# Kernel optimization log

Measured on AMD Instinct MI355X. Metric: run time of the kernel, lower is better.

The kernel has to match this reference:

```python
import jax, jax.numpy as jnp
import numpy as np

B, N, DIM, H = 2, 2048, 1024, 16
D = DIM // H  # head_dim = 64


def setup_inputs() -> dict:
    key = jax.random.key(0)
    ks = jax.random.split(key, 3)
    w_scale = 0.02
    return {
        "x": jax.random.normal(ks[0], (B, N, DIM), dtype=jnp.float32),
        "Wqkv": jax.random.normal(ks[1], (DIM, 3 * DIM), dtype=jnp.float32) * w_scale,
        "bqkv": jnp.zeros((3 * DIM,), dtype=jnp.float32),
        "Wproj": jax.random.normal(ks[2], (DIM, DIM), dtype=jnp.float32) * w_scale,
        "bproj": jnp.zeros((DIM,), dtype=jnp.float32),
        "sigma": jnp.ones((1,), dtype=jnp.float32),
        "gamma": jnp.ones((1,), dtype=jnp.float32),
    }


def reference(x, Wqkv, bqkv, Wproj, bproj, sigma, gamma):
    b, n, c = x.shape
    # qkv projection -> (B, N, 3, H, D)
    qkv = (x @ Wqkv + bqkv).reshape(b, n, 3, H, D)
    q = jnp.transpose(qkv[:, :, 0], (0, 2, 1, 3))  # [B, H, N, D]
    k = jnp.transpose(qkv[:, :, 1], (0, 2, 1, 3))
    v = jnp.transpose(qkv[:, :, 2], (0, 2, 1, 3))
    scale = 1.0 / jnp.sqrt(jnp.asarray(D, dtype=x.dtype))
    scores = jnp.einsum("bhqd,bhkd->bhqk", q, k) * scale  # [B, H, N, N]
    # divisive normalization (cortical gain control) over key axis
    denom = sigma + jnp.sqrt(jnp.mean(scores * scores, axis=-1, keepdims=True))
    scores = gamma * scores / denom
    attn = jax.nn.softmax(scores, axis=-1)
    out = jnp.einsum("bhqk,bhkd->bhqd", attn, v)  # [B, H, N, D]
    out = jnp.transpose(out, (0, 2, 1, 3)).reshape(b, n, c)
    return out @ Wproj + bproj
```

## Files before the change

### kernel.cpp

```cpp
#include <hip/hip_runtime.h>

typedef __attribute__((ext_vector_type(4))) float f32x4;
typedef __attribute__((ext_vector_type(8))) _Float16 f16x8;
typedef __attribute__((ext_vector_type(4))) _Float16 f16x4;
typedef __attribute__((ext_vector_type(2))) _Float16 f16x2;

#define MFMA_F16(a, b, c) __builtin_amdgcn_mfma_f32_16x16x32_f16(a, b, c, 0, 0, 0)

__device__ __forceinline__ void gload_lds16(const void* g, void* l) {
  __builtin_amdgcn_global_load_lds(
      (const __attribute__((address_space(1))) void*)g,
      (__attribute__((address_space(3))) void*)l, 16, 0, 0);
}
__device__ __forceinline__ f16x2 pk2(float a, float b) {
  return __builtin_bit_cast(f16x2, __builtin_amdgcn_cvt_pkrtz(a, b));
}
__device__ __forceinline__ void pipe_barrier_v4() {
  asm volatile("s_waitcnt vmcnt(4) lgkmcnt(0)" ::: "memory");
  __builtin_amdgcn_sched_barrier(0);
  __builtin_amdgcn_s_barrier();
}
__device__ __forceinline__ void pipe_barrier_v3() {
  asm volatile("s_waitcnt vmcnt(3) lgkmcnt(0)" ::: "memory");
  __builtin_amdgcn_sched_barrier(0);
  __builtin_amdgcn_s_barrier();
}
__device__ __forceinline__ void pipe_barrier_v2() {
  asm volatile("s_waitcnt vmcnt(2) lgkmcnt(0)" ::: "memory");
  __builtin_amdgcn_sched_barrier(0);
  __builtin_amdgcn_s_barrier();
}
__device__ __forceinline__ void pipe_barrier_v0() {
  asm volatile("s_waitcnt vmcnt(0) lgkmcnt(0)" ::: "memory");
  __builtin_amdgcn_sched_barrier(0);
  __builtin_amdgcn_s_barrier();
}

__global__ __launch_bounds__(256) void prep_kernel(
    const float* __restrict__ x, _Float16* __restrict__ xf,
    const float* __restrict__ Wqkv, _Float16* __restrict__ wqt,
    const float* __restrict__ Wproj, _Float16* __restrict__ wpt) {
  __shared__ float tile[32][33];
  const int bx = blockIdx.x;
  if (bx < 4096) {
    const int i = bx * 256 + threadIdx.x;
    f32x4 v = *(const f32x4*)(x + (size_t)i * 4);
    f16x4 h;
#pragma unroll
    for (int j = 0; j < 4; ++j) h[j] = (_Float16)v[j];
    *(f16x4*)(xf + (size_t)i * 4) = h;
    return;
  }
  const float* W;
  _Float16* wt;
  int N, n0, k0;
  if (bx < 7168) {
    const int t = bx - 4096;
    W = Wqkv; wt = wqt; N = 3072;
    n0 = (t % 96) * 32; k0 = (t / 96) * 32;
  } else {
    const int t = bx - 7168;
    W = Wproj; wt = wpt; N = 1024;
    n0 = (t % 32) * 32; k0 = (t / 32) * 32;
  }
  const int tx = threadIdx.x & 31, ty = threadIdx.x >> 5;
#pragma unroll
  for (int j = 0; j < 32; j += 8)
    tile[ty + j][tx] = W[(size_t)(k0 + ty + j) * N + n0 + tx];
  __syncthreads();
#pragma unroll
  for (int j = 0; j < 32; j += 8)
    wt[(size_t)(n0 + ty + j) * 1024 + k0 + tx] = (_Float16)tile[tx][ty + j];
}

__global__ __launch_bounds__(256) void gemm_qkv_kernel(
    const _Float16* __restrict__ xf, const _Float16* __restrict__ wt,
    const float* __restrict__ bias, _Float16* __restrict__ QF,
    _Float16* __restrict__ KF, _Float16* __restrict__ KT,
    _Float16* __restrict__ VT) {
  __shared__ __attribute__((aligned(16))) _Float16 lg[24576];
  const int tid = threadIdx.x, lane = tid & 63, w = tid >> 6;
  const int wg = blockIdx.x;
  const int cx = wg & 7, c = wg >> 3;
  const int bxl = (cx & 1) * 12 + c % 12;
  const int byl = (cx >> 1) * 8 + c / 12;
  const int m0 = byl * 128, n0 = bxl * 128;
  const int wr = (w >> 1) * 64, wc = (w & 1) * 64;
  f32x4 acc[4][4] = {};

  const int srow = lane >> 2;
  const int scol = (((lane & 3) ^ ((lane >> 3) & 3)) * 8);
  const int fr = lane & 15, fg = lane >> 4;
  const int rswz = (fr >> 1) & 3;

  auto stageT = [&](int buf, int k0) {
#pragma unroll
    for (int j = 0; j < 2; ++j) {
      const int rbase = 32 * w + 16 * j;
      const int r = rbase + srow;
      gload_lds16(xf + (size_t)(m0 + r) * 1024 + k0 + scol,
                  &lg[buf * 8192 + rbase * 32]);
      gload_lds16(wt + (size_t)(n0 + r) * 1024 + k0 + scol,
                  &lg[buf * 8192 + 4096 + rbase * 32]);
    }
  };

  stageT(0, 0);
  stageT(1, 32);
  pipe_barrier_v4();
  int cur = 0;
  for (int t = 0; t < 32; ++t) {
    if (t < 30) {
      const int nb = (cur + 2 >= 3) ? cur - 1 : cur + 2;
      stageT(nb, (t + 2) * 32);
    }
    const int ab = cur * 8192;
    f16x8 af[4], bfr[4];
#pragma unroll
    for (int m = 0; m < 4; ++m)
      af[m] = *(const f16x8*)&lg[ab + (wr + 16 * m + fr) * 32 + ((fg ^ rswz) * 8)];
#pragma unroll
    for (int n = 0; n < 4; ++n)
      bfr[n] = *(const f16x8*)&lg[ab + 4096 + (wc + 16 * n + fr) * 32 + ((fg ^ rswz) * 8)];
#pragma unroll
    for (int m = 0; m < 4; ++m)
#pragma unroll
      for (int n = 0; n < 4; ++n) acc[m][n] = MFMA_F16(af[m], bfr[n], acc[m][n]);
    if (t < 30) pipe_barrier_v4(); else pipe_barrier_v0();
    cur = (cur + 1 == 3) ? 0 : cur + 1;
  }

  const int fq = fg * 4;
#pragma unroll
  for (int n = 0; n < 4; ++n) {
    const float bv = bias[n0 + wc + 16 * n + fr];
#pragma unroll
    for (int m = 0; m < 4; ++m)
#pragma unroll
      for (int i = 0; i < 4; ++i)
        lg[(wr + 16 * m + fq + i) * 129 + wc + 16 * n + fr] =
            (_Float16)(acc[m][n][i] + bv);
  }
  __syncthreads();
  const int b = m0 >> 11, nnb = m0 & 2047;
  const int h0 = 2 * (bxl & 7);
  const int sPhase = bxl >> 3;
  if (sPhase <= 1) {
    _Float16* __restrict__ dst = (sPhase == 0) ? QF : KF;
#pragma unroll
    for (int p = 0; p < 8; ++p) {
      const int r = p * 16 + (tid >> 4);
      const int cc = tid & 15;
      f16x8 vals;
#pragma unroll
      for (int j = 0; j < 8; ++j) vals[j] = lg[r * 129 + cc * 8 + j];
      const int h = cc >> 3, d = (cc & 7) * 8;
      *(f16x8*)&dst[((size_t)((b * 16 + h0 + h) * 2048 + nnb + r)) * 64 + d] = vals;
    }
  }
  if (sPhase >= 1) {
    _Float16* __restrict__ T = (sPhase == 1) ? KT : VT;
#pragma unroll
    for (int p = 0; p < 8; ++p) {
      const int lr = p * 16 + (tid >> 4);
      const int cc = tid & 15;
      f16x8 vals;
#pragma unroll
      for (int j = 0; j < 8; ++j) vals[j] = lg[(cc * 8 + j) * 129 + lr];
      const int h = lr >> 6, d = lr & 63;
      *(f16x8*)&T[((size_t)((b * 16 + h0 + h) * 64 + d)) * 2048 + nnb + cc * 8] = vals;
    }
  }
}

__global__ __launch_bounds__(256) void gram_kernel(
    const _Float16* __restrict__ KT, _Float16* __restrict__ GH,
    _Float16* __restrict__ GL) {
  __shared__ __attribute__((aligned(16))) _Float16 sT[3][4096];
  const int tid = threadIdx.x, lane = tid & 63, w = tid >> 6;
  const int bh = blockIdx.x;
  const _Float16* src = KT + (size_t)bh * 64 * 2048;
  const int s_r = lane >> 3, s_cg = lane & 7;
  const int fr = lane & 15, fg = lane >> 4;
  const int kswz = fr & 7;

  auto stage = [&](int buf, int n0) {
#pragma unroll
    for (int j = 0; j < 2; ++j) {
      const int rbase = 8 * w + 32 * j;
      gload_lds16(src + (size_t)(rbase + s_r) * 2048 + n0 + ((s_cg ^ s_r) * 8),
                  &sT[buf][rbase * 64]);
    }
  };

  f32x4 acc[4] = {};
  stage(0, 0);
  stage(1, 64);
  pipe_barrier_v2();
  int cur = 0;
  for (int t = 0; t < 32; ++t) {
    if (t < 30) {
      const int nb = (cur + 2 >= 3) ? cur - 1 : cur + 2;
      stage(nb, (t + 2) * 64);
    }
    f16x8 af[2];
#pragma unroll
    for (int ks = 0; ks < 2; ++ks)
      af[ks] = *(const f16x8*)&sT[cur][(16 * w + fr) * 64 + (((ks * 4 + fg) ^ kswz) * 8)];
#pragma unroll
    for (int nt = 0; nt < 4; ++nt)
#pragma unroll
      for (int ks = 0; ks < 2; ++ks)
        acc[nt] = MFMA_F16(
            af[ks],
            *(const f16x8*)&sT[cur][(16 * nt + fr) * 64 + (((ks * 4 + fg) ^ kswz) * 8)],
            acc[nt]);
    if (t < 30) pipe_barrier_v2(); else pipe_barrier_v0();
    cur = (cur + 1 == 3) ? 0 : cur + 1;
  }
#pragma unroll
  for (int nt = 0; nt < 4; ++nt) {
#pragma unroll
    for (int i = 0; i < 4; ++i) {
      const float g = acc[nt][i];
      const _Float16 gh = (_Float16)g;
      const size_t o = (size_t)bh * 4096 + (16 * w + fg * 4 + i) * 64 + 16 * nt + fr;
      GH[o] = gh;
      GL[o] = (_Float16)(g - (float)gh);
    }
  }
}

__global__ __launch_bounds__(256) void attn_kernel(
    const _Float16* __restrict__ QF, const _Float16* __restrict__ KF,
    const _Float16* __restrict__ VT, const _Float16* __restrict__ GH,
    const _Float16* __restrict__ GL, _Float16* __restrict__ OB,
    const float* __restrict__ sigma_p, const float* __restrict__ gamma_p) {
  __shared__ __attribute__((aligned(16))) _Float16 lds[32768];

  const int tid = threadIdx.x, lane = tid & 63, w = tid >> 6;
  const int wg = blockIdx.x;
  const int c = wg >> 3;
  const int bh = (wg & 7) * 4 + (c >> 4);
  const int q0 = (c & 15) * 128;
  const size_t base = (size_t)bh * (2048 * 64);
  const float sigma = sigma_p[0], gamma = gamma_p[0];
  const int fr = lane & 15, fg = lane >> 4;
  const int s_r = lane >> 3, s_cg = lane & 7;
  const int kswz = fr & 7;

  const _Float16* Kbh = KF + base;
  const _Float16* Tbh = VT + base;

  f16x8 qf[2][2];
#pragma unroll
  for (int m = 0; m < 2; ++m)
#pragma unroll
    for (int ks = 0; ks < 2; ++ks)
      qf[m][ks] = *(const f16x8*)(QF + base +
                                  (size_t)(q0 + 32 * w + 16 * m + fr) * 64 +
                                  ks * 32 + fg * 8);

  auto stage64 = [&](int dstoff, const _Float16* g, int srcstride) {
#pragma unroll
    for (int j = 0; j < 2; ++j) {
      const int rbase = 8 * w + 32 * j;
      gload_lds16(g + (size_t)(rbase + s_r) * srcstride + ((s_cg ^ s_r) * 8),
                  &lds[dstoff + rbase * 64]);
    }
  };
  auto stage64K = [&](int dstoff, const _Float16* g) {
#pragma unroll
    for (int j = 0; j < 2; ++j) {
      const int rbase = 8 * w + 32 * j;
      const int r = rbase + s_r;
      const int pr = (r & 0x23) | ((r & 0x0C) << 1) | ((r & 0x10) >> 2);
      gload_lds16(g + (size_t)pr * 64 + ((s_cg ^ s_r) * 8),
                  &lds[dstoff + rbase * 64]);
    }
  };

  stage64(0, GH + (size_t)bh * 4096, 64);
  stage64(4096, GL + (size_t)bh * 4096, 64);
  __syncthreads();
  float minvl2[2];
  float* Yp = (float*)&lds[8192 + w * 2048];
#pragma unroll
  for (int m = 0; m < 2; ++m) {
    f32x4 yacc[4] = {};
#pragma unroll
    for (int nt = 0; nt < 4; ++nt) {
#pragma unroll
      for (int ks = 0; ks < 2; ++ks) {
        const int off = (16 * nt + fr) * 64 + (((ks * 4 + fg) ^ kswz) * 8);
        yacc[nt] = MFMA_F16(qf[m][ks], *(const f16x8*)&lds[off], yacc[nt]);
        yacc[nt] = MFMA_F16(qf[m][ks], *(const f16x8*)&lds[4096 + off], yacc[nt]);
      }
    }
#pragma unroll
    for (int nt = 0; nt < 4; ++nt)
#pragma unroll
      for (int i = 0; i < 4; ++i) Yp[(fg * 4 + i) * 64 + 16 * nt + fr] = yacc[nt][i];
    float zp = 0.0f;
#pragma unroll
    for (int ks = 0; ks < 2; ++ks) {
      const f32x4 y0 = *(const f32x4*)&Yp[fr * 64 + ks * 32 + fg * 8];
      const f32x4 y1 = *(const f32x4*)&Yp[fr * 64 + ks * 32 + fg * 8 + 4];
#pragma unroll
      for (int cc = 0; cc < 4; ++cc) {
        zp += y0[cc] * (float)qf[m][ks][cc];
        zp += y1[cc] * (float)qf[m][ks][cc + 4];
      }
    }
    zp += __shfl_xor(zp, 16);
    zp += __shfl_xor(zp, 32);
    const float rms = sqrtf(fmaxf(zp, 0.0f)) * (1.0f / 362.038672f);
    minvl2[m] = gamma / (sigma + rms) * 0.125f * 1.44269504f;
  }
  __syncthreads();

  float lsum[2] = {};
  f32x4 oacc[2][4] = {};
  stage64K(0, Kbh);
  stage64(16384, Tbh, 2048);
  stage64K(4096, Kbh + 4096);
  stage64(20480, Tbh + 64, 2048);
  pipe_barrier_v0();
  for (int g = 0; g < 16; ++g) {
    if (g < 15) {
      const int qb = ((g + 1) & 1) * 2;
      const int t2 = 2 * g + 2;
      stage64K(qb * 4096, Kbh + (size_t)t2 * 4096);
      stage64(16384 + qb * 4096, Tbh + t2 * 64, 2048);
      stage64K((qb + 1) * 4096, Kbh + (size_t)(t2 + 1) * 4096);
      stage64(16384 + (qb + 1) * 4096, Tbh + (t2 + 1) * 64, 2048);
    }
    const int pb = (g & 1) * 2;
#pragma unroll
    for (int tt = 0; tt < 2; ++tt) {
      const int koff = (pb + tt) * 4096, voff = 16384 + (pb + tt) * 4096;
      f32x4 pacc[2][4];
      __builtin_amdgcn_s_setprio(1);
#pragma unroll
      for (int n = 0; n < 4; ++n) {
        const int offb = koff + (16 * n + fr) * 64;
        const f16x8 kf0 = *(const f16x8*)&lds[offb + ((fg ^ kswz) * 8)];
        const f16x8 kf1 = *(const f16x8*)&lds[offb + (((4 + fg) ^ kswz) * 8)];
#pragma unroll
        for (int m = 0; m < 2; ++m) {
          f32x4 a = {};
          a = MFMA_F16(kf0, qf[m][0], a);
          a = MFMA_F16(kf1, qf[m][1], a);
          pacc[m][n] = a;
        }
      }
      __builtin_amdgcn_s_setprio(0);
#pragma unroll
      for (int m = 0; m < 2; ++m)
#pragma unroll
        for (int n = 0; n < 4; ++n)
#pragma unroll
          for (int i = 0; i < 4; ++i) {
            const float p = __builtin_amdgcn_exp2f(pacc[m][n][i] * minvl2[m]);
            lsum[m] += p;
            pacc[m][n][i] = p;
          }
#pragma unroll
      for (int ks2 = 0; ks2 < 2; ++ks2) {
        f16x8 bf[2];
#pragma unroll
        for (int m = 0; m < 2; ++m) {
          const f16x2 c0 = pk2(pacc[m][2 * ks2][0], pacc[m][2 * ks2][1]);
          const f16x2 c1 = pk2(pacc[m][2 * ks2][2], pacc[m][2 * ks2][3]);
          const f16x2 c2 = pk2(pacc[m][2 * ks2 + 1][0], pacc[m][2 * ks2 + 1][1]);
          const f16x2 c3 = pk2(pacc[m][2 * ks2 + 1][2], pacc[m][2 * ks2 + 1][3]);
          bf[m][0] = c0[0]; bf[m][1] = c0[1]; bf[m][2] = c1[0]; bf[m][3] = c1[1];
          bf[m][4] = c2[0]; bf[m][5] = c2[1]; bf[m][6] = c3[0]; bf[m][7] = c3[1];
        }
        __builtin_amdgcn_s_setprio(1);
#pragma unroll
        for (int nf = 0; nf < 4; ++nf) {
          const int off = voff + (16 * nf + fr) * 64 + (((ks2 * 4 + fg) ^ kswz) * 8);
          const f16x8 vt = *(const f16x8*)&lds[off];
          oacc[0][nf] = MFMA_F16(vt, bf[0], oacc[0][nf]);
          oacc[1][nf] = MFMA_F16(vt, bf[1], oacc[1][nf]);
        }
        __builtin_amdgcn_s_setprio(0);
      }
    }
    pipe_barrier_v0();
  }
  float inv[2];
#pragma unroll
  for (int m = 0; m < 2; ++m) {
    lsum[m] += __shfl_xor(lsum[m], 16);
    lsum[m] += __shfl_xor(lsum[m], 32);
    inv[m] = 1.0f / lsum[m];
  }

  const int b = bh >> 4, h = bh & 15;
#pragma unroll
  for (int m = 0; m < 2; ++m) {
    const size_t orow = (size_t)(b * 2048 + q0 + 32 * w + 16 * m + fr);
#pragma unroll
    for (int nf = 0; nf < 4; ++nf) {
      f16x4 ov;
#pragma unroll
      for (int i = 0; i < 4; ++i) ov[i] = (_Float16)(oacc[m][nf][i] * inv[m]);
      *(f16x4*)&OB[orow * 1024 + h * 64 + 16 * nf + 4 * fg] = ov;
    }
  }
}

__global__ __launch_bounds__(256) void gemm_proj_kernel(
    const _Float16* __restrict__ A, const _Float16* __restrict__ Bt,
    const float* __restrict__ bias, float* __restrict__ out) {
  __shared__ __attribute__((aligned(16))) _Float16 lg[18432];
  const int tid = threadIdx.x, lane = tid & 63, w = tid >> 6;
  const int wg = blockIdx.x;
  const int c = wg >> 3;
  const int bxl = c & 7;
  const int byl = (wg & 7) * 8 + (c >> 3);
  const int m0 = byl * 64, n0 = bxl * 128;
  const int wr = (w >> 1) * 32, wc = (w & 1) * 64;
  f32x4 acc[2][4] = {};
  const int srow = lane >> 2;
  const int scol = (((lane & 3) ^ ((lane >> 3) & 3)) * 8);
  const int fr = lane & 15, fg = lane >> 4;
  const int rswz = (fr >> 1) & 3;

  auto stageT = [&](int buf, int k0) {
    {
      const int rbase = 16 * w;
      gload_lds16(A + (size_t)(m0 + rbase + srow) * 1024 + k0 + scol,
                  &lg[buf * 6144 + rbase * 32]);
    }
#pragma unroll
    for (int j = 0; j < 2; ++j) {
      const int rbase = 32 * w + 16 * j;
      gload_lds16(Bt + (size_t)(n0 + rbase + srow) * 1024 + k0 + scol,
                  &lg[buf * 6144 + 2048 + rbase * 32]);
    }
  };

  stageT(0, 0);
  stageT(1, 32);
  pipe_barrier_v3();
  int cur = 0;
  for (int t = 0; t < 32; ++t) {
    if (t < 30) {
      const int nb = (cur + 2 >= 3) ? cur - 1 : cur + 2;
      stageT(nb, (t + 2) * 32);
    }
    const int ab = cur * 6144;
    f16x8 af[2], bfr[4];
#pragma unroll
    for (int m = 0; m < 2; ++m)
      af[m] = *(const f16x8*)&lg[ab + (wr + 16 * m + fr) * 32 + ((fg ^ rswz) * 8)];
#pragma unroll
    for (int n = 0; n < 4; ++n)
      bfr[n] = *(const f16x8*)&lg[ab + 2048 + (wc + 16 * n + fr) * 32 + ((fg ^ rswz) * 8)];
#pragma unroll
    for (int m = 0; m < 2; ++m)
#pragma unroll
      for (int n = 0; n < 4; ++n) acc[m][n] = MFMA_F16(af[m], bfr[n], acc[m][n]);
    if (t < 30) pipe_barrier_v3(); else pipe_barrier_v0();
    cur = (cur + 1 == 3) ? 0 : cur + 1;
  }
  const int fq = fg * 4;
#pragma unroll
  for (int n = 0; n < 4; ++n) {
    const int col = n0 + wc + 16 * n + fr;
    const float bv = bias[col];
#pragma unroll
    for (int m = 0; m < 2; ++m) {
#pragma unroll
      for (int i = 0; i < 4; ++i) {
        const int row = m0 + wr + 16 * m + fq + i;
        out[(size_t)row * 1024 + col] = acc[m][n][i] + bv;
      }
    }
  }
}

extern "C" void kernel_launch(void* const* d_in, const int* in_sizes, int n_in,
                              void* d_out, int out_size, void* d_ws, size_t ws_size,
                              hipStream_t stream) {
  const float* x = (const float*)d_in[0];
  const float* Wqkv = (const float*)d_in[1];
  const float* bqkv = (const float*)d_in[2];
  const float* Wproj = (const float*)d_in[3];
  const float* bproj = (const float*)d_in[4];
  const float* sigma = (const float*)d_in[5];
  const float* gamma = (const float*)d_in[6];
  float* out = (float*)d_out;

  char* ws = (char*)d_ws;
  const size_t MB = 1024 * 1024;
  _Float16* XF  = (_Float16*)(ws + 0 * MB);
  _Float16* WQT = (_Float16*)(ws + 8 * MB);
  _Float16* WPT = (_Float16*)(ws + 14 * MB);
  _Float16* QF  = (_Float16*)(ws + 16 * MB);
  _Float16* KF  = (_Float16*)(ws + 24 * MB);
  _Float16* VT  = (_Float16*)(ws + 32 * MB);
  _Float16* KT  = (_Float16*)(ws + 40 * MB);
  _Float16* OB  = (_Float16*)(ws + 40 * MB);
  _Float16* GH  = (_Float16*)(ws + 8 * MB);
  _Float16* GL  = (_Float16*)(ws + 8 * MB + 512 * 1024);

  prep_kernel<<<8192, 256, 0, stream>>>(x, XF, Wqkv, WQT, Wproj, WPT);
  gemm_qkv_kernel<<<768, 256, 0, stream>>>(XF, WQT, bqkv, QF, KF, KT, VT);
  gram_kernel<<<32, 256, 0, stream>>>(KT, GH, GL);
  attn_kernel<<<512, 256, 0, stream>>>(QF, KF, VT, GH, GL, OB, sigma, gamma);
  gemm_proj_kernel<<<512, 256, 0, stream>>>(OB, WPT, bproj, out);
}
```

Before: 128.0 us.

## Split Gram computation across blocks and software-pipeline QK/PV in attention

The Gram-matrix kernel, which used only 32 blocks, is split into 128 blocks that each cover a quarter of the sequence and write fp32 partials. A small reduce kernel sums them and emits the hi/lo fp16 split. The attention loop is restructured to a triple-buffered single-tile pipeline, where the QK MFMA for the next tile is issued before the PV of the current tile, letting exp/pack overlap matrix work. This adds a kernel launch and extra partial traffic, and uses less LDS per block.

```diff
diff --git a/kernel.cpp b/kernel.cpp
--- a/kernel.cpp
+++ b/kernel.cpp
@@ -173,13 +173,12 @@
   }
 }
 
-__global__ __launch_bounds__(256) void gram_kernel(
-    const _Float16* __restrict__ KT, _Float16* __restrict__ GH,
-    _Float16* __restrict__ GL) {
+__global__ __launch_bounds__(256) void gram_partial_kernel(
+    const _Float16* __restrict__ KT, float* __restrict__ GP) {
   __shared__ __attribute__((aligned(16))) _Float16 sT[3][4096];
   const int tid = threadIdx.x, lane = tid & 63, w = tid >> 6;
-  const int bh = blockIdx.x;
-  const _Float16* src = KT + (size_t)bh * 64 * 2048;
+  const int bh = blockIdx.x >> 2, qt = blockIdx.x & 3;
+  const _Float16* src = KT + (size_t)bh * 64 * 2048 + qt * 512;
   const int s_r = lane >> 3, s_cg = lane & 7;
   const int fr = lane & 15, fg = lane >> 4;
   const int kswz = fr & 7;
@@ -198,8 +197,8 @@
   stage(1, 64);
   pipe_barrier_v2();
   int cur = 0;
-  for (int t = 0; t < 32; ++t) {
-    if (t < 30) {
+  for (int t = 0; t < 8; ++t) {
+    if (t < 6) {
       const int nb = (cur + 2 >= 3) ? cur - 1 : cur + 2;
       stage(nb, (t + 2) * 64);
     }
@@ -215,20 +214,35 @@
             af[ks],
             *(const f16x8*)&sT[cur][(16 * nt + fr) * 64 + (((ks * 4 + fg) ^ kswz) * 8)],
             acc[nt]);
-    if (t < 30) pipe_barrier_v2(); else pipe_barrier_v0();
+    if (t < 6) pipe_barrier_v2(); else pipe_barrier_v0();
     cur = (cur + 1 == 3) ? 0 : cur + 1;
   }
-#pragma unroll
-  for (int nt = 0; nt < 4; ++nt) {
-#pragma unroll
-    for (int i = 0; i < 4; ++i) {
-      const float g = acc[nt][i];
-      const _Float16 gh = (_Float16)g;
-      const size_t o = (size_t)bh * 4096 + (16 * w + fg * 4 + i) * 64 + 16 * nt + fr;
-      GH[o] = gh;
-      GL[o] = (_Float16)(g - (float)gh);
-    }
-  }
+  float* dst = GP + (size_t)blockIdx.x * 4096;
+#pragma unroll
+  for (int nt = 0; nt < 4; ++nt)
+#pragma unroll
+    for (int i = 0; i < 4; ++i)
+      dst[(16 * w + fg * 4 + i) * 64 + 16 * nt + fr] = acc[nt][i];
+}
+
+__global__ __launch_bounds__(256) void gram_reduce_kernel(
+    const float* __restrict__ GP, _Float16* __restrict__ GH,
+    _Float16* __restrict__ GL) {
+  const int bh = blockIdx.x >> 2, seg = blockIdx.x & 3;
+  const int e0 = seg * 1024 + threadIdx.x * 4;
+  const float* p = GP + (size_t)bh * 4 * 4096 + e0;
+  f32x4 s = *(const f32x4*)p;
+  s += *(const f32x4*)(p + 4096);
+  s += *(const f32x4*)(p + 8192);
+  s += *(const f32x4*)(p + 12288);
+  f16x4 gh, gl;
+#pragma unroll
+  for (int j = 0; j < 4; ++j) {
+    gh[j] = (_Float16)s[j];
+    gl[j] = (_Float16)(s[j] - (float)gh[j]);
+  }
+  *(f16x4*)&GH[(size_t)bh * 4096 + e0] = gh;
+  *(f16x4*)&GL[(size_t)bh * 4096 + e0] = gl;
 }
 
 __global__ __launch_bounds__(256) void attn_kernel(
@@ -236,7 +250,7 @@
     const _Float16* __restrict__ VT, const _Float16* __restrict__ GH,
     const _Float16* __restrict__ GL, _Float16* __restrict__ OB,
     const float* __restrict__ sigma_p, const float* __restrict__ gamma_p) {
-  __shared__ __attribute__((aligned(16))) _Float16 lds[32768];
+  __shared__ __attribute__((aligned(16))) _Float16 lds[24576];
 
   const int tid = threadIdx.x, lane = tid & 63, w = tid >> 6;
   const int wg = blockIdx.x;
@@ -321,75 +335,96 @@
 
   float lsum[2] = {};
   f32x4 oacc[2][4] = {};
+
+  auto qk_tile = [&](int kbuf, f32x4 (&pn)[2][4]) {
+#pragma unroll
+    for (int n = 0; n < 4; ++n) {
+      const int offb = kbuf * 4096 + (16 * n + fr) * 64;
+      const f16x8 kf0 = *(const f16x8*)&lds[offb + ((fg ^ kswz) * 8)];
+      const f16x8 kf1 = *(const f16x8*)&lds[offb + (((4 + fg) ^ kswz) * 8)];
+#pragma unroll
+      for (int m = 0; m < 2; ++m) {
+        f32x4 a = {};
+        a = MFMA_F16(kf0, qf[m][0], a);
+        a = MFMA_F16(kf1, qf[m][1], a);
+        pn[m][n] = a;
+      }
+    }
+  };
+  auto exp_pack = [&](f32x4 (&pn)[2][4], f16x8 (&pa)[2][2]) {
+#pragma unroll
+    for (int m = 0; m < 2; ++m) {
+#pragma unroll
+      for (int n = 0; n < 4; ++n)
+#pragma unroll
+        for (int i = 0; i < 4; ++i) {
+          const float p = __builtin_amdgcn_exp2f(pn[m][n][i] * minvl2[m]);
+          lsum[m] += p;
+          pn[m][n][i] = p;
+        }
+#pragma unroll
+      for (int k2 = 0; k2 < 2; ++k2) {
+        const f16x2 c0 = pk2(pn[m][2 * k2][0], pn[m][2 * k2][1]);
+        const f16x2 c1 = pk2(pn[m][2 * k2][2], pn[m][2 * k2][3]);
+        const f16x2 c2 = pk2(pn[m][2 * k2 + 1][0], pn[m][2 * k2 + 1][1]);
+        const f16x2 c3 = pk2(pn[m][2 * k2 + 1][2], pn[m][2 * k2 + 1][3]);
+        pa[m][k2][0] = c0[0]; pa[m][k2][1] = c0[1];
+        pa[m][k2][2] = c1[0]; pa[m][k2][3] = c1[1];
+        pa[m][k2][4] = c2[0]; pa[m][k2][5] = c2[1];
+        pa[m][k2][6] = c3[0]; pa[m][k2][7] = c3[1];
+      }
+    }
+  };
+  auto pv_tile = [&](int vbuf, f16x8 (&pa)[2][2]) {
+#pragma unroll
+    for (int k2 = 0; k2 < 2; ++k2) {
+#pragma unroll
+      for (int nf = 0; nf < 4; ++nf) {
+        const int off = 12288 + vbuf * 4096 + (16 * nf + fr) * 64 +
+                        (((k2 * 4 + fg) ^ kswz) * 8);
+        const f16x8 vt = *(const f16x8*)&lds[off];
+        oacc[0][nf] = MFMA_F16(vt, pa[0][k2], oacc[0][nf]);
+        oacc[1][nf] = MFMA_F16(vt, pa[1][k2], oacc[1][nf]);
+      }
+    }
+  };
+
   stage64K(0, Kbh);
-  stage64(16384, Tbh, 2048);
+  stage64(12288, Tbh, 2048);
   stage64K(4096, Kbh + 4096);
-  stage64(20480, Tbh + 64, 2048);
+  stage64(16384, Tbh + 64, 2048);
   pipe_barrier_v0();
-  for (int g = 0; g < 16; ++g) {
-    if (g < 15) {
-      const int qb = ((g + 1) & 1) * 2;
-      const int t2 = 2 * g + 2;
-      stage64K(qb * 4096, Kbh + (size_t)t2 * 4096);
-      stage64(16384 + qb * 4096, Tbh + t2 * 64, 2048);
-      stage64K((qb + 1) * 4096, Kbh + (size_t)(t2 + 1) * 4096);
-      stage64(16384 + (qb + 1) * 4096, Tbh + (t2 + 1) * 64, 2048);
-    }
-    const int pb = (g & 1) * 2;
-#pragma unroll
-    for (int tt = 0; tt < 2; ++tt) {
-      const int koff = (pb + tt) * 4096, voff = 16384 + (pb + tt) * 4096;
-      f32x4 pacc[2][4];
+
+  f32x4 pn[2][4];
+  f16x8 pa[2][2], pan[2][2];
+  qk_tile(0, pn);
+  exp_pack(pn, pa);
+
+  for (int t = 0; t < 32; ++t) {
+    const int cb = t % 3;
+    if (t < 30) {
+      const int sb = (t + 2) % 3;
+      stage64K(sb * 4096, Kbh + (size_t)(t + 2) * 4096);
+      stage64(12288 + sb * 4096, Tbh + (t + 2) * 64, 2048);
+    }
+    if (t < 31) {
       __builtin_amdgcn_s_setprio(1);
-#pragma unroll
-      for (int n = 0; n < 4; ++n) {
-        const int offb = koff + (16 * n + fr) * 64;
-        const f16x8 kf0 = *(const f16x8*)&lds[offb + ((fg ^ kswz) * 8)];
-        const f16x8 kf1 = *(const f16x8*)&lds[offb + (((4 + fg) ^ kswz) * 8)];
-#pragma unroll
-        for (int m = 0; m < 2; ++m) {
-          f32x4 a = {};
-          a = MFMA_F16(kf0, qf[m][0], a);
-          a = MFMA_F16(kf1, qf[m][1], a);
-          pacc[m][n] = a;
-        }
-      }
+      qk_tile((t + 1) % 3, pn);
       __builtin_amdgcn_s_setprio(0);
+    }
+    __builtin_amdgcn_s_setprio(1);
+    pv_tile(cb, pa);
+    __builtin_amdgcn_s_setprio(0);
+    if (t < 31) {
+      exp_pack(pn, pan);
 #pragma unroll
       for (int m = 0; m < 2; ++m)
 #pragma unroll
-        for (int n = 0; n < 4; ++n)
-#pragma unroll
-          for (int i = 0; i < 4; ++i) {
-            const float p = __builtin_amdgcn_exp2f(pacc[m][n][i] * minvl2[m]);
-            lsum[m] += p;
-            pacc[m][n][i] = p;
-          }
-#pragma unroll
-      for (int ks2 = 0; ks2 < 2; ++ks2) {
-        f16x8 bf[2];
-#pragma unroll
-        for (int m = 0; m < 2; ++m) {
-          const f16x2 c0 = pk2(pacc[m][2 * ks2][0], pacc[m][2 * ks2][1]);
-          const f16x2 c1 = pk2(pacc[m][2 * ks2][2], pacc[m][2 * ks2][3]);
-          const f16x2 c2 = pk2(pacc[m][2 * ks2 + 1][0], pacc[m][2 * ks2 + 1][1]);
-          const f16x2 c3 = pk2(pacc[m][2 * ks2 + 1][2], pacc[m][2 * ks2 + 1][3]);
-          bf[m][0] = c0[0]; bf[m][1] = c0[1]; bf[m][2] = c1[0]; bf[m][3] = c1[1];
-          bf[m][4] = c2[0]; bf[m][5] = c2[1]; bf[m][6] = c3[0]; bf[m][7] = c3[1];
-        }
-        __builtin_amdgcn_s_setprio(1);
-#pragma unroll
-        for (int nf = 0; nf < 4; ++nf) {
-          const int off = voff + (16 * nf + fr) * 64 + (((ks2 * 4 + fg) ^ kswz) * 8);
-          const f16x8 vt = *(const f16x8*)&lds[off];
-          oacc[0][nf] = MFMA_F16(vt, bf[0], oacc[0][nf]);
-          oacc[1][nf] = MFMA_F16(vt, bf[1], oacc[1][nf]);
-        }
-        __builtin_amdgcn_s_setprio(0);
-      }
-    }
-    pipe_barrier_v0();
-  }
+        for (int k2 = 0; k2 < 2; ++k2) pa[m][k2] = pan[m][k2];
+      pipe_barrier_v0();
+    }
+  }
+
   float inv[2];
 #pragma unroll
   for (int m = 0; m < 2; ++m) {
@@ -507,10 +542,12 @@
   _Float16* OB  = (_Float16*)(ws + 40 * MB);
   _Float16* GH  = (_Float16*)(ws + 8 * MB);
   _Float16* GL  = (_Float16*)(ws + 8 * MB + 512 * 1024);
+  float*    GP  = (float*)(ws + 9 * MB);
 
   prep_kernel<<<8192, 256, 0, stream>>>(x, XF, Wqkv, WQT, Wproj, WPT);
   gemm_qkv_kernel<<<768, 256, 0, stream>>>(XF, WQT, bqkv, QF, KF, KT, VT);
-  gram_kernel<<<32, 256, 0, stream>>>(KT, GH, GL);
+  gram_partial_kernel<<<128, 256, 0, stream>>>(KT, GP);
+  gram_reduce_kernel<<<128, 256, 0, stream>>>(GP, GH, GL);
   attn_kernel<<<512, 256, 0, stream>>>(QF, KF, VT, GH, GL, OB, sigma, gamma);
   gemm_proj_kernel<<<512, 256, 0, stream>>>(OB, WPT, bproj, out);
 }
```

Measured after the change: 124.6 us. -2.7%, faster.
